# Performance work log

Hardware: AMD Instinct MI355X
Metric: run time of the kernel (lower is better)

## Reference

```python
import jax, jax.numpy as jnp
import numpy as np

B_SZ = 512; S = 3; F = 5; C = 62; E = 5
D_MODEL = C * E * F          # 1550
N_LAYERS = 2
D_STATE = 16
EXPAND = 2
D_CONV = 4
ED = EXPAND * D_MODEL        # 3100
DT_RANK = (D_MODEL + 15) // 16  # 97
VOCAB = 128
EPS = 1e-5


def setup_inputs() -> dict:
    key = jax.random.key(0)
    ks = jax.random.split(key, 10)
    def g(i, shape, scale=0.02):
        return jax.random.normal(ks[i], shape, dtype=jnp.float32) * scale
    A_log = jnp.tile(jnp.log(jnp.arange(1, D_STATE + 1, dtype=jnp.float32))[None, None, :],
                     (N_LAYERS, ED, 1))
    return {
        "x": jax.random.normal(ks[0], (B_SZ, S, F, C, E), dtype=jnp.float32),
        "in_proj_w": g(1, (N_LAYERS, 2 * ED, D_MODEL)),
        "conv_w": g(2, (N_LAYERS, ED, 1, D_CONV), 0.1),
        "conv_b": jnp.zeros((N_LAYERS, ED), jnp.float32),
        "x_proj_w": g(3, (N_LAYERS, DT_RANK + 2 * D_STATE, ED)),
        "dt_proj_w": g(4, (N_LAYERS, ED, DT_RANK), 0.1),
        "dt_proj_b": jnp.full((N_LAYERS, ED), -4.6, jnp.float32),  # softplus ~ 0.01
        "A_log": A_log,
        "D_param": jnp.ones((N_LAYERS, ED), jnp.float32),
        "out_proj_w": g(5, (N_LAYERS, D_MODEL, ED)),
        "norm_w": jnp.ones((N_LAYERS, D_MODEL), jnp.float32),
        "normf_w": jnp.ones((D_MODEL,), jnp.float32),
        "lm_head_w": g(6, (VOCAB, D_MODEL)),
        "bn_w": jnp.ones((F,), jnp.float32),
        "bn_b": jnp.zeros((F,), jnp.float32),
        "emb_w": g(7, (256, VOCAB)),
        "emb_b": jnp.zeros((256,), jnp.float32),
    }


def _rmsnorm(x, w):
    return x * jax.lax.rsqrt(jnp.mean(x * x, axis=-1, keepdims=True) + EPS) * w


def _silu(x):
    return x * jax.nn.sigmoid(x)


def _causal_conv(xt, w, b):
    # xt: (B, ED, L); w: (ED, 1, K) depthwise causal conv (pad K-1 left)
    y = jax.lax.conv_general_dilated(xt, w, (1,), [(D_CONV - 1, 0)],
                                     feature_group_count=ED)
    return y + b[None, :, None]


def _ssm_scan(deltaA, deltaBx, Cm):
    # deltaA, deltaBx: (B, L, ED, N); Cm: (B, L, N)
    def step(h, inp):
        dA, dBx, c = inp
        h = dA * h + dBx                      # (B, ED, N)
        y = jnp.einsum('ben,bn->be', h, c)    # (B, ED)
        return h, y
    h0 = jnp.zeros((deltaA.shape[0], ED, D_STATE), deltaA.dtype)
    xs = (deltaA.transpose(1, 0, 2, 3), deltaBx.transpose(1, 0, 2, 3), Cm.transpose(1, 0, 2))
    _, ys = jax.lax.scan(step, h0, xs)
    return ys.transpose(1, 0, 2)              # (B, L, ED)


def _mixer(h, in_w, cw, cb, xp_w, dt_w, dt_b, A_log, Dp, out_w):
    # h: (B, L, D_MODEL)
    xz = jnp.einsum('bld,ed->ble', h, in_w)   # (B, L, 2*ED)
    x_in, z = jnp.split(xz, 2, axis=-1)
    xc = _silu(_causal_conv(x_in.transpose(0, 2, 1), cw, cb).transpose(0, 2, 1))  # (B,L,ED)
    dbc = jnp.einsum('ble,re->blr', xc, xp_w)  # (B, L, DT_RANK + 2N)
    dt = dbc[..., :DT_RANK]
    Bm = dbc[..., DT_RANK:DT_RANK + D_STATE]
    Cm = dbc[..., DT_RANK + D_STATE:]
    delta = jax.nn.softplus(jnp.einsum('blr,er->ble', dt, dt_w) + dt_b)  # (B,L,ED)
    A = -jnp.exp(A_log)                       # (ED, N)
    deltaA = jnp.exp(delta[..., None] * A)                       # (B,L,ED,N)
    deltaBx = delta[..., None] * Bm[:, :, None, :] * xc[..., None]
    y = _ssm_scan(deltaA, deltaBx, Cm) + Dp * xc
    return jnp.einsum('ble,de->bld', y * _silu(z), out_w)


def reference(x, in_proj_w, conv_w, conv_b, x_proj_w, dt_proj_w, dt_proj_b,
              A_log, D_param, out_proj_w, norm_w, normf_w, lm_head_w,
              bn_w, bn_b, emb_w, emb_b):
    b, s, f, c, e = x.shape
    fx = x.transpose(0, 1, 3, 2, 4).reshape(b, s, c * f * e)  # (B, S, D_MODEL)
    h = fx
    for l in range(N_LAYERS):
        h = h + _mixer(_rmsnorm(h, norm_w[l]), in_proj_w[l], conv_w[l], conv_b[l],
                       x_proj_w[l], dt_proj_w[l], dt_proj_b[l], A_log[l],
                       D_param[l], out_proj_w[l])
    h = _rmsnorm(h, normf_w)
    logits = jnp.einsum('bsd,vd->bsv', h, lm_head_w)          # (B, S, 128)
    m = jnp.broadcast_to(logits[:, None], (b, f, s, VOCAB))    # repeat over f
    # BatchNorm2d(feature_dim) in training mode: stats over (B, S, VOCAB) per channel f
    mean = jnp.mean(m, axis=(0, 2, 3), keepdims=True)
    var = jnp.var(m, axis=(0, 2, 3), keepdims=True)
    mn = (m - mean) * jax.lax.rsqrt(var + EPS)
    mn = mn * bn_w[None, :, None, None] + bn_b[None, :, None, None]
    return jnp.einsum('bfsv,ov->bfso', mn, emb_w) + emb_b      # (B, F, S, 256)
```

## Files before the change

kernel.cpp:

```cpp
#include <hip/hip_runtime.h>
#include <hip/hip_bf16.h>
#include <math.h>

#define B_SZ 512
#define SEQ 3
#define D_MODEL 1550
#define ED 3100
#define NSTATE 16
#define DTR 97
#define DBC_R 129
#define VOCAB 128
#define NBS (B_SZ*SEQ)
#define EPSV 1e-5f

#define KD 1600
#define KE 3136
#define NIP 6272
#define NXP 256
#define NOP 1664
#define NDT 3200
#define KDT 128
#define DBC_LD 256

#define QIP 2508800
#define QXP 200704
#define QDT 102400
#define QOP 1304576
#define AEL 49600
#define QLM 51200
#define TEL 32768
#define PREP_N1 4166080
#define PREP_N0 4250306

static inline int cdiv_h(int a, int b){ return (a + b - 1) / b; }

__device__ __forceinline__ float silu_f(float x){ return x / (1.0f + expf(-x)); }

using bf16x8 = __attribute__((ext_vector_type(8))) short;
using f32x4  = __attribute__((ext_vector_type(4))) float;

__device__ __forceinline__ void gload16(const void* g, void* l){
  __builtin_amdgcn_global_load_lds(
      (const __attribute__((address_space(1))) unsigned int*)g,
      (__attribute__((address_space(3))) unsigned int*)l,
      16, 0, 0);
}

__global__ void k_permute(const float* __restrict__ x, float* __restrict__ h){
  int idx = blockIdx.x * 256 + threadIdx.x;
  if (idx >= NBS * D_MODEL) return;
  int d = idx % D_MODEL;
  int row = idx / D_MODEL;
  int e = d % 5;
  int f = (d / 5) % 5;
  int c = d / 25;
  h[idx] = x[(((size_t)row * 5 + f) * 62 + c) * 5 + e];
}

__device__ __forceinline__ void cast4(const float* __restrict__ src,
                                      __hip_bfloat16* __restrict__ dst,
                                      int q, int N, int K, int Kp){
  int i4 = q * 4;
  int row = i4 / Kp;
  int col = i4 % Kp;
  const float* srow = src + (size_t)row * K;
  #pragma unroll
  for (int j = 0; j < 4; j++){
    int c = col + j;
    float v = (row < N && c < K) ? srow[c] : 0.f;
    dst[i4 + j] = __float2bfloat16(v);
  }
}

__global__ __launch_bounds__(256)
void k_prep(const float* __restrict__ ipw, const float* __restrict__ xpw,
            const float* __restrict__ dtw, const float* __restrict__ opw,
            const float* __restrict__ alog,
            const float* __restrict__ lmw, const float* __restrict__ embw,
            __hip_bfloat16* __restrict__ ipb, __hip_bfloat16* __restrict__ xpb,
            __hip_bfloat16* __restrict__ dtwb, __hip_bfloat16* __restrict__ opb,
            float* __restrict__ A_t,
            __hip_bfloat16* __restrict__ lmb,
            float* __restrict__ emb_t, float* __restrict__ sumw,
            float* __restrict__ stats, int l0){
  int idx = blockIdx.x * 256 + threadIdx.x;
  if (idx < QIP){ cast4(ipw, ipb, idx, 2 * ED, D_MODEL, KD); return; } idx -= QIP;
  if (idx < QXP){ cast4(xpw, xpb, idx, DBC_R, ED, KE); return; } idx -= QXP;
  if (idx < QDT){ cast4(dtw, dtwb, idx, ED, DTR, KDT); return; } idx -= QDT;
  if (idx < QOP){ cast4(opw, opb, idx, D_MODEL, ED, KE); return; } idx -= QOP;
  if (idx < AEL){
    int n = idx / ED, ch = idx % ED;
    A_t[idx] = -expf(alog[(size_t)ch * NSTATE + n]);
    return;
  } idx -= AEL;
  if (!l0) return;
  if (idx < QLM){ cast4(lmw, lmb, idx, VOCAB, D_MODEL, KD); return; } idx -= QLM;
  if (idx < TEL){
    int v = idx >> 8, o = idx & 255;
    emb_t[idx] = embw[(size_t)o * VOCAB + v];
    return;
  } idx -= TEL;
  if (idx < 256){
    const float* r = embw + (size_t)idx * VOCAB;
    float s = 0.f;
    for (int v = 0; v < VOCAB; v++) s += r[v];
    sumw[idx] = s;
    return;
  } idx -= 256;
  if (idx < 2) stats[idx] = 0.f;
}

__global__ void k_rmsnorm_bf16(const float* __restrict__ in, const float* __restrict__ w,
                               __hip_bfloat16* __restrict__ out, int D, int Kp){
  int row = blockIdx.x;
  const float* xr = in + (size_t)row * D;
  float ss = 0.f;
  for (int i = threadIdx.x; i < D; i += blockDim.x){ float v = xr[i]; ss = fmaf(v, v, ss); }
  __shared__ float red[4];
  __shared__ float sscale;
  int lane = threadIdx.x & 63, wv = threadIdx.x >> 6;
  #pragma unroll
  for (int o = 32; o > 0; o >>= 1) ss += __shfl_down(ss, o, 64);
  if (lane == 0) red[wv] = ss;
  __syncthreads();
  if (threadIdx.x == 0){
    float t = red[0] + red[1] + red[2] + red[3];
    sscale = 1.0f / sqrtf(t / (float)D + EPSV);
  }
  __syncthreads();
  float sc = sscale;
  __hip_bfloat16* orow = out + (size_t)row * Kp;
  for (int i = threadIdx.x; i < Kp; i += blockDim.x){
    float v = (i < D) ? xr[i] * sc * w[i] : 0.f;
    orow[i] = __float2bfloat16(v);
  }
}

template<int SPLITS, bool ATOMIC, bool OUT_BF16, bool PARTIAL>
__global__ __launch_bounds__(256)
void k_gemm2(const __hip_bfloat16* __restrict__ A, const __hip_bfloat16* __restrict__ B,
             void* Cv, int Kp, int Nld, int Nreal){
  __shared__ short Al[2][4096];
  __shared__ short Bl[2][4096];
  const int gx = gridDim.x, gy = gridDim.y;
  const int nwg = gx * gy;
  const int wg = blockIdx.y * gx + blockIdx.x;
  const int q = nwg >> 3, r = nwg & 7;
  const int xcd = wg & 7, off = wg >> 3;
  const int nid = (xcd < r ? xcd * (q + 1) : r * (q + 1) + (xcd - r) * q) + off;
  const int bm = (nid % gy) * 128;
  const int bn = (nid / gy) * 128;

  const int t = threadIdx.x;
  const int tt8 = t * 8;

  int kb = 0, ke = Kp;
  if (SPLITS > 1){
    int Kc = ((Kp / SPLITS + 31) / 32) * 32;
    kb = blockIdx.z * Kc;
    ke = min(kb + Kc, Kp);
    if (kb >= ke) return;
  }
  const int nt = (ke - kb) / 32;

  const int cg = ((t & 3) ^ ((t >> 2) & 3)) * 8;
  const short* Ab = (const short*)A;
  const short* Bb = (const short*)B;
  const short* ga0 = Ab + (size_t)(bm + (t >> 2)) * Kp + cg;
  const short* ga1 = Ab + (size_t)(bm + 64 + (t >> 2)) * Kp + cg;
  const short* gb0 = Bb + (size_t)(bn + (t >> 2)) * Kp + cg;
  const short* gb1 = Bb + (size_t)(bn + 64 + (t >> 2)) * Kp + cg;

  const int l = t & 63;
  const int wid = t >> 6;
  const int wr = wid >> 1, wc = wid & 1;
  const int fr = l & 15;
  const int cc = ((l >> 4) ^ (l & 3)) * 8;

  f32x4 acc[4][4] = {};

#define STAGE(buf, kof) do{ \
    gload16(ga0 + (kof), &Al[buf][tt8]); \
    gload16(ga1 + (kof), &Al[buf][2048 + tt8]); \
    gload16(gb0 + (kof), &Bl[buf][tt8]); \
    gload16(gb1 + (kof), &Bl[buf][2048 + tt8]); }while(0)

  STAGE(0, kb);
  __syncthreads();
  int cur = 0;
  for (int it = 0; it < nt; ++it){
    if (it + 1 < nt) STAGE(cur ^ 1, kb + (it + 1) * 32);
    bf16x8 af[4], bfr[4];
    #pragma unroll
    for (int m = 0; m < 4; m++)
      af[m] = *(const bf16x8*)&Al[cur][(wr * 64 + m * 16 + fr) * 32 + cc];
    #pragma unroll
    for (int n = 0; n < 4; n++)
      bfr[n] = *(const bf16x8*)&Bl[cur][(wc * 64 + n * 16 + fr) * 32 + cc];
    #pragma unroll
    for (int m = 0; m < 4; m++)
      #pragma unroll
      for (int n = 0; n < 4; n++)
        acc[m][n] = __builtin_amdgcn_mfma_f32_16x16x32_bf16(af[m], bfr[n], acc[m][n], 0, 0, 0);
    if (it + 1 < nt){ __syncthreads(); cur ^= 1; }
  }
#undef STAGE

  float* Cf = (float*)Cv;
  __hip_bfloat16* Cb = (__hip_bfloat16*)Cv;
  const size_t pstride = (size_t)gy * 128 * Nld;
  if (PARTIAL) Cf += (size_t)blockIdx.z * pstride;
  const int r0 = (l >> 4) * 4;
  #pragma unroll
  for (int m = 0; m < 4; m++){
    #pragma unroll
    for (int n = 0; n < 4; n++){
      int col = bn + wc * 64 + n * 16 + fr;
      if (col < Nreal){
        size_t base = (size_t)(bm + wr * 64 + m * 16 + r0) * Nld + col;
        #pragma unroll
        for (int j = 0; j < 4; j++){
          float v = acc[m][n][j];
          size_t o = base + (size_t)j * Nld;
          if (OUT_BF16)      Cb[o] = __float2bfloat16(v);
          else if (ATOMIC)   atomicAdd(&Cf[o], v);
          else               Cf[o] = v;
        }
      }
    }
  }
}

__global__ void k_conv_silu(const __hip_bfloat16* __restrict__ xz, const float* __restrict__ cw,
                            const float* __restrict__ cb, __hip_bfloat16* __restrict__ xc_b){
  int idx = blockIdx.x * 256 + threadIdx.x;
  if (idx >= B_SZ * KE) return;
  int ch = idx % KE;
  int b  = idx / KE;
  size_t ob = (size_t)b * SEQ * KE + ch;
  if (ch >= ED){
    __hip_bfloat16 z = __float2bfloat16(0.f);
    xc_b[ob] = z; xc_b[ob + KE] = z; xc_b[ob + 2 * KE] = z;
    return;
  }
  const __hip_bfloat16* base = xz + (size_t)b * SEQ * NIP + ch;
  float x0 = __bfloat162float(base[0]);
  float x1 = __bfloat162float(base[NIP]);
  float x2 = __bfloat162float(base[2 * NIP]);
  const float* w = cw + (size_t)ch * 4;
  float w1 = w[1], w2 = w[2], w3 = w[3];
  float bb = cb[ch];
  float s0 = silu_f(fmaf(w3, x0, bb));
  float s1 = silu_f(fmaf(w2, x0, fmaf(w3, x1, bb)));
  float s2 = silu_f(fmaf(w1, x0, fmaf(w2, x1, fmaf(w3, x2, bb))));
  xc_b[ob]          = __float2bfloat16(s0);
  xc_b[ob + KE]     = __float2bfloat16(s1);
  xc_b[ob + 2 * KE] = __float2bfloat16(s2);
}

__global__ __launch_bounds__(256)
void k_xred(const float* __restrict__ part, float* __restrict__ dbc,
            __hip_bfloat16* __restrict__ dbc_b){
  int idx = blockIdx.x * 256 + threadIdx.x;
  if (idx >= NBS * DBC_LD) return;
  float s = 0.f;
  #pragma unroll
  for (int p = 0; p < 8; p++) s += part[(size_t)p * NBS * DBC_LD + idx];
  dbc[idx] = s;
  int c = idx & 255, row = idx >> 8;
  if (c < KDT) dbc_b[(size_t)row * KDT + c] = __float2bfloat16(c < DTR ? s : 0.f);
}

__global__ __launch_bounds__(256)
void k_scan2(const __hip_bfloat16* __restrict__ delta_b, const float* __restrict__ dbc,
             const float* __restrict__ dtb, const float* __restrict__ A_t,
             const float* __restrict__ Dp, const __hip_bfloat16* __restrict__ xz,
             __hip_bfloat16* __restrict__ xc_b){
  __shared__ float sB[SEQ][NSTATE], sC[SEQ][NSTATE];
  int b = blockIdx.y;
  if (threadIdx.x < SEQ * 2 * NSTATE){
    int t = threadIdx.x / (2 * NSTATE), r = threadIdx.x % (2 * NSTATE);
    float v = dbc[(size_t)(b * SEQ + t) * DBC_LD + DTR + r];
    if (r < NSTATE) sB[t][r] = v; else sC[t][r - NSTATE] = v;
  }
  __syncthreads();
  int ch = blockIdx.x * 256 + threadIdx.x;
  if (ch >= ED) return;

  float bias = dtb[ch];
  float dlt[SEQ];
  #pragma unroll
  for (int t = 0; t < SEQ; t++){
    float acc = __bfloat162float(delta_b[(size_t)(b * SEQ + t) * NDT + ch]) + bias;
    dlt[t] = (acc > 20.f) ? acc : log1pf(expf(acc));
  }

  size_t ob = (size_t)b * SEQ * KE + ch;
  float xcv[SEQ] = { __bfloat162float(xc_b[ob]),
                     __bfloat162float(xc_b[ob + KE]),
                     __bfloat162float(xc_b[ob + 2 * KE]) };
  float y[SEQ] = {0.f, 0.f, 0.f};
  #pragma unroll
  for (int n = 0; n < NSTATE; n++){
    float Av = A_t[(size_t)n * ED + ch];
    float hs = 0.f;
    #pragma unroll
    for (int t = 0; t < SEQ; t++){
      float dA = expf(dlt[t] * Av);
      hs = fmaf(dA, hs, dlt[t] * sB[t][n] * xcv[t]);
      y[t] = fmaf(hs, sC[t][n], y[t]);
    }
  }
  float dp = Dp[ch];
  const __hip_bfloat16* zbase = xz + (size_t)b * SEQ * NIP + ED + ch;
  #pragma unroll
  for (int t = 0; t < SEQ; t++){
    float z = __bfloat162float(zbase[(size_t)t * NIP]);
    float yy = fmaf(dp, xcv[t], y[t]);
    xc_b[ob + (size_t)t * KE] = __float2bfloat16(yy * silu_f(z));
  }
}

__global__ __launch_bounds__(256)
void k_statsred(const float* __restrict__ part, float* __restrict__ logits,
                float* __restrict__ stats){
  float s = 0.f, ss = 0.f;
  for (int i = blockIdx.x * 256 + threadIdx.x; i < NBS * VOCAB; i += gridDim.x * 256){
    float v = 0.f;
    #pragma unroll
    for (int p = 0; p < 4; p++) v += part[(size_t)p * NBS * VOCAB + i];
    logits[i] = v;
    s += v; ss = fmaf(v, v, ss);
  }
  #pragma unroll
  for (int o = 32; o > 0; o >>= 1){ s += __shfl_down(s, o, 64); ss += __shfl_down(ss, o, 64); }
  __shared__ float rs[4], rss[4];
  int lane = threadIdx.x & 63, wv = threadIdx.x >> 6;
  if (lane == 0){ rs[wv] = s; rss[wv] = ss; }
  __syncthreads();
  if (threadIdx.x == 0){
    atomicAdd(&stats[0], rs[0] + rs[1] + rs[2] + rs[3]);
    atomicAdd(&stats[1], rss[0] + rss[1] + rss[2] + rss[3]);
  }
}

__global__ __launch_bounds__(256)
void k_projfinal(const float* __restrict__ logits, const float* __restrict__ emb_t,
                 const float* __restrict__ sumw, const float* __restrict__ stats,
                 const float* __restrict__ bnw, const float* __restrict__ bnb,
                 const float* __restrict__ embb, float* __restrict__ out){
  __shared__ float row[VOCAB];
  int r = blockIdx.x;
  int o = threadIdx.x;
  if (o < VOCAB) row[o] = logits[(size_t)r * VOCAB + o];
  __syncthreads();
  float p = 0.f;
  #pragma unroll 8
  for (int v = 0; v < VOCAB; v++) p = fmaf(row[v], emb_t[v * 256 + o], p);
  const float invN = 1.0f / (float)(NBS * VOCAB);
  float mean = stats[0] * invN;
  float var  = stats[1] * invN - mean * mean;
  float rstd = rsqrtf(var + EPSV);
  int b = r / SEQ, s = r % SEQ;
  float sw = sumw[o];
  float base = rstd * (p - mean * sw);
  float eb = embb[o];
  #pragma unroll
  for (int f = 0; f < 5; f++){
    out[(((size_t)(b * 5 + f)) * SEQ + s) * 256 + o] = bnw[f] * base + bnb[f] * sw + eb;
  }
}

extern "C" void kernel_launch(void* const* d_in, const int* in_sizes, int n_in,
                              void* d_out, int out_size, void* d_ws, size_t ws_size,
                              hipStream_t stream) {
  const float* x          = (const float*)d_in[0];
  const float* in_proj_w  = (const float*)d_in[1];
  const float* conv_w     = (const float*)d_in[2];
  const float* conv_b     = (const float*)d_in[3];
  const float* x_proj_w   = (const float*)d_in[4];
  const float* dt_proj_w  = (const float*)d_in[5];
  const float* dt_proj_b  = (const float*)d_in[6];
  const float* A_log      = (const float*)d_in[7];
  const float* D_param    = (const float*)d_in[8];
  const float* out_proj_w = (const float*)d_in[9];
  const float* norm_w     = (const float*)d_in[10];
  const float* normf_w    = (const float*)d_in[11];
  const float* lm_head_w  = (const float*)d_in[12];
  const float* bn_w       = (const float*)d_in[13];
  const float* bn_b       = (const float*)d_in[14];
  const float* emb_w      = (const float*)d_in[15];
  const float* emb_b      = (const float*)d_in[16];

  float* ws = (float*)d_ws;
  float* h      = ws;
  float* dbc    = h      + (size_t)NBS * D_MODEL;
  float* logits = dbc    + (size_t)NBS * DBC_LD;
  float* sumw   = logits + (size_t)NBS * VOCAB;
  float* stats  = sumw   + 256;
  float* A_t    = stats  + 2;
  float* emb_t  = A_t    + (size_t)NSTATE * ED;
  float* xpart  = emb_t  + (size_t)VOCAB * 256;
  float* lmpart = xpart  + (size_t)8 * NBS * DBC_LD;
  __hip_bfloat16* xz_b   = (__hip_bfloat16*)(lmpart + (size_t)4 * NBS * VOCAB);
  __hip_bfloat16* hn_b   = xz_b   + (size_t)NBS * NIP;
  __hip_bfloat16* xc_b   = hn_b   + (size_t)NBS * KD;
  __hip_bfloat16* dbc_b  = xc_b   + (size_t)NBS * KE;
  __hip_bfloat16* dlt_b  = dbc_b  + (size_t)NBS * KDT;
  __hip_bfloat16* ipb    = dlt_b  + (size_t)NBS * NDT;
  __hip_bfloat16* xpb    = ipb    + (size_t)NIP * KD;
  __hip_bfloat16* dtwb   = xpb    + (size_t)NXP * KE;
  __hip_bfloat16* opb    = dtwb   + (size_t)NDT * KDT;
  __hip_bfloat16* lmb    = opb    + (size_t)NOP * KE;
  size_t need = (size_t)((char*)(lmb + (size_t)VOCAB * KD) - (char*)ws);
  if (ws_size < need) return;

  k_permute<<<cdiv_h(NBS * D_MODEL, 256), 256, 0, stream>>>(x, h);

  for (int l = 0; l < 2; l++){
    const float* ipw = in_proj_w  + (size_t)l * 2 * ED * D_MODEL;
    const float* cw  = conv_w     + (size_t)l * ED * 4;
    const float* cb  = conv_b     + (size_t)l * ED;
    const float* xpw = x_proj_w   + (size_t)l * DBC_R * ED;
    const float* dtw = dt_proj_w  + (size_t)l * ED * DTR;
    const float* dtb = dt_proj_b  + (size_t)l * ED;
    const float* al  = A_log      + (size_t)l * ED * NSTATE;
    const float* dp  = D_param    + (size_t)l * ED;
    const float* opw = out_proj_w + (size_t)l * D_MODEL * ED;
    const float* nw  = norm_w     + (size_t)l * D_MODEL;

    k_prep<<<cdiv_h(l == 0 ? PREP_N0 : PREP_N1, 256), 256, 0, stream>>>(
        ipw, xpw, dtw, opw, al, lm_head_w, emb_w,
        ipb, xpb, dtwb, opb, A_t, lmb, emb_t, sumw, stats, l == 0 ? 1 : 0);

    k_rmsnorm_bf16<<<NBS, 256, 0, stream>>>(h, nw, hn_b, D_MODEL, KD);

    k_gemm2<1, false, true, false><<<dim3(NIP / 128, NBS / 128, 1), 256, 0, stream>>>(
        hn_b, ipb, xz_b, KD, NIP, NIP);

    k_conv_silu<<<cdiv_h(B_SZ * KE, 256), 256, 0, stream>>>(xz_b, cw, cb, xc_b);

    k_gemm2<8, false, false, true><<<dim3(NXP / 128, NBS / 128, 8), 256, 0, stream>>>(
        xc_b, xpb, xpart, KE, DBC_LD, DBC_LD);
    k_xred<<<cdiv_h(NBS * DBC_LD, 256), 256, 0, stream>>>(xpart, dbc, dbc_b);

    k_gemm2<1, false, true, false><<<dim3(NDT / 128, NBS / 128, 1), 256, 0, stream>>>(
        dbc_b, dtwb, dlt_b, KDT, NDT, NDT);

    k_scan2<<<dim3(cdiv_h(ED, 256), B_SZ), 256, 0, stream>>>(
        dlt_b, dbc, dtb, A_t, dp, xz_b, xc_b);

    k_gemm2<4, true, false, false><<<dim3(NOP / 128, NBS / 128, 4), 256, 0, stream>>>(
        xc_b, opb, h, KE, D_MODEL, D_MODEL);
  }

  k_rmsnorm_bf16<<<NBS, 256, 0, stream>>>(h, normf_w, hn_b, D_MODEL, KD);
  k_gemm2<4, false, false, true><<<dim3(1, NBS / 128, 4), 256, 0, stream>>>(
      hn_b, lmb, lmpart, KD, VOCAB, VOCAB);
  k_statsred<<<192, 256, 0, stream>>>(lmpart, logits, stats);

  k_projfinal<<<NBS, 256, 0, stream>>>(logits, emb_t, sumw, stats,
                                       bn_w, bn_b, emb_b, (float*)d_out);
}
```

Before: 570.3 us.

## Replace atomic split-K out_proj with bf16 partials and a reduction kernel

The out_proj split-K GEMM no longer does fp32 atomicAdd into the residual. It now writes bf16 partial tiles, and a new k_ored kernel sums the four partials into h. The partial buffers share one workspace region, and the weight cast now writes four bf16 values with a single vector store. This removes atomic contention and traffic at the cost of an extra launch and extra partial reads and writes, and it rounds the partial sums to bf16, which adds error.

```diff
diff --git a/kernel.cpp b/kernel.cpp
--- a/kernel.cpp
+++ b/kernel.cpp
@@ -46,6 +46,11 @@
       16, 0, 0);
 }
 
+__device__ __forceinline__ unsigned short bfbits(float v){
+  __hip_bfloat16 b = __float2bfloat16(v);
+  return *(unsigned short*)&b;
+}
+
 __global__ void k_permute(const float* __restrict__ x, float* __restrict__ h){
   int idx = blockIdx.x * 256 + threadIdx.x;
   if (idx >= NBS * D_MODEL) return;
@@ -64,12 +69,12 @@
   int row = i4 / Kp;
   int col = i4 % Kp;
   const float* srow = src + (size_t)row * K;
-  #pragma unroll
-  for (int j = 0; j < 4; j++){
-    int c = col + j;
-    float v = (row < N && c < K) ? srow[c] : 0.f;
-    dst[i4 + j] = __float2bfloat16(v);
-  }
+  ushort4 o;
+  o.x = bfbits((row < N && col + 0 < K) ? srow[col + 0] : 0.f);
+  o.y = bfbits((row < N && col + 1 < K) ? srow[col + 1] : 0.f);
+  o.z = bfbits((row < N && col + 2 < K) ? srow[col + 2] : 0.f);
+  o.w = bfbits((row < N && col + 3 < K) ? srow[col + 3] : 0.f);
+  *(ushort4*)(dst + i4) = o;
 }
 
 __global__ __launch_bounds__(256)
@@ -136,7 +141,7 @@
   }
 }
 
-template<int SPLITS, bool ATOMIC, bool OUT_BF16, bool PARTIAL>
+template<int SPLITS, bool OUT_BF16, bool PARTIAL>
 __global__ __launch_bounds__(256)
 void k_gemm2(const __hip_bfloat16* __restrict__ A, const __hip_bfloat16* __restrict__ B,
              void* Cv, int Kp, int Nld, int Nreal){
@@ -208,8 +213,11 @@
 
   float* Cf = (float*)Cv;
   __hip_bfloat16* Cb = (__hip_bfloat16*)Cv;
-  const size_t pstride = (size_t)gy * 128 * Nld;
-  if (PARTIAL) Cf += (size_t)blockIdx.z * pstride;
+  if (PARTIAL){
+    const size_t pstride = (size_t)gy * 128 * Nld;
+    if (OUT_BF16) Cb += (size_t)blockIdx.z * pstride;
+    else          Cf += (size_t)blockIdx.z * pstride;
+  }
   const int r0 = (l >> 4) * 4;
   #pragma unroll
   for (int m = 0; m < 4; m++){
@@ -222,9 +230,8 @@
         for (int j = 0; j < 4; j++){
           float v = acc[m][n][j];
           size_t o = base + (size_t)j * Nld;
-          if (OUT_BF16)      Cb[o] = __float2bfloat16(v);
-          else if (ATOMIC)   atomicAdd(&Cf[o], v);
-          else               Cf[o] = v;
+          if (OUT_BF16) Cb[o] = __float2bfloat16(v);
+          else          Cf[o] = v;
         }
       }
     }
@@ -269,6 +276,17 @@
   dbc[idx] = s;
   int c = idx & 255, row = idx >> 8;
   if (c < KDT) dbc_b[(size_t)row * KDT + c] = __float2bfloat16(c < DTR ? s : 0.f);
+}
+
+__global__ __launch_bounds__(256)
+void k_ored(const __hip_bfloat16* __restrict__ part, float* __restrict__ h){
+  int idx = blockIdx.x * 256 + threadIdx.x;
+  if (idx >= NBS * D_MODEL) return;
+  float s = h[idx];
+  #pragma unroll
+  for (int p = 0; p < 4; p++)
+    s += __bfloat162float(part[(size_t)p * NBS * D_MODEL + idx]);
+  h[idx] = s;
 }
 
 __global__ __launch_bounds__(256)
@@ -400,9 +418,12 @@
   float* stats  = sumw   + 256;
   float* A_t    = stats  + 2;
   float* emb_t  = A_t    + (size_t)NSTATE * ED;
-  float* xpart  = emb_t  + (size_t)VOCAB * 256;
-  float* lmpart = xpart  + (size_t)8 * NBS * DBC_LD;
-  __hip_bfloat16* xz_b   = (__hip_bfloat16*)(lmpart + (size_t)4 * NBS * VOCAB);
+  float* spart  = emb_t  + (size_t)VOCAB * 256;
+  size_t spart_f = ((size_t)4 * NBS * D_MODEL * 2 + 3) / 4;
+  float* xpart  = spart;
+  float* lmpart = spart;
+  __hip_bfloat16* opart = (__hip_bfloat16*)spart;
+  __hip_bfloat16* xz_b   = (__hip_bfloat16*)(spart + spart_f);
   __hip_bfloat16* hn_b   = xz_b   + (size_t)NBS * NIP;
   __hip_bfloat16* xc_b   = hn_b   + (size_t)NBS * KD;
   __hip_bfloat16* dbc_b  = xc_b   + (size_t)NBS * KE;
@@ -435,27 +456,28 @@
 
     k_rmsnorm_bf16<<<NBS, 256, 0, stream>>>(h, nw, hn_b, D_MODEL, KD);
 
-    k_gemm2<1, false, true, false><<<dim3(NIP / 128, NBS / 128, 1), 256, 0, stream>>>(
+    k_gemm2<1, true, false><<<dim3(NIP / 128, NBS / 128, 1), 256, 0, stream>>>(
         hn_b, ipb, xz_b, KD, NIP, NIP);
 
     k_conv_silu<<<cdiv_h(B_SZ * KE, 256), 256, 0, stream>>>(xz_b, cw, cb, xc_b);
 
-    k_gemm2<8, false, false, true><<<dim3(NXP / 128, NBS / 128, 8), 256, 0, stream>>>(
+    k_gemm2<8, false, true><<<dim3(NXP / 128, NBS / 128, 8), 256, 0, stream>>>(
         xc_b, xpb, xpart, KE, DBC_LD, DBC_LD);
     k_xred<<<cdiv_h(NBS * DBC_LD, 256), 256, 0, stream>>>(xpart, dbc, dbc_b);
 
-    k_gemm2<1, false, true, false><<<dim3(NDT / 128, NBS / 128, 1), 256, 0, stream>>>(
+    k_gemm2<1, true, false><<<dim3(NDT / 128, NBS / 128, 1), 256, 0, stream>>>(
         dbc_b, dtwb, dlt_b, KDT, NDT, NDT);
 
     k_scan2<<<dim3(cdiv_h(ED, 256), B_SZ), 256, 0, stream>>>(
         dlt_b, dbc, dtb, A_t, dp, xz_b, xc_b);
 
-    k_gemm2<4, true, false, false><<<dim3(NOP / 128, NBS / 128, 4), 256, 0, stream>>>(
-        xc_b, opb, h, KE, D_MODEL, D_MODEL);
+    k_gemm2<4, true, true><<<dim3(NOP / 128, NBS / 128, 4), 256, 0, stream>>>(
+        xc_b, opb, opart, KE, D_MODEL, D_MODEL);
+    k_ored<<<cdiv_h(NBS * D_MODEL, 256), 256, 0, stream>>>(opart, h);
   }
 
   k_rmsnorm_bf16<<<NBS, 256, 0, stream>>>(h, normf_w, hn_b, D_MODEL, KD);
-  k_gemm2<4, false, false, true><<<dim3(1, NBS / 128, 4), 256, 0, stream>>>(
+  k_gemm2<4, false, true><<<dim3(1, NBS / 128, 4), 256, 0, stream>>>(
       hn_b, lmb, lmpart, KD, VOCAB, VOCAB);
   k_statsred<<<192, 256, 0, stream>>>(lmpart, logits, stats);
 
```

Measured after the change: 497.8 us. 12.7% less time.
